# Kernel tuning notes

Hardware: AMD Instinct MI355X
Metric: run time of the kernel (lower is better)

The kernel has to match this reference:

```python
import jax, jax.numpy as jnp
import numpy as np

MAX_OBJECTS = 20
NODE_FEAT_DIM = 16
HID = 256
N_OPS = 8
N_COLORS = 10
B = 16384
EPS = 1e-5


def _ln(x, g, b):
    m = x.mean(-1, keepdims=True)
    v = ((x - m) ** 2).mean(-1, keepdims=True)
    return (x - m) / jnp.sqrt(v + EPS) * g + b


def _mlp(x, w1, b1, w2, b2):
    return jax.nn.relu(x @ w1 + b1) @ w2 + b2


def setup_inputs() -> dict:
    key = jax.random.key(0)
    ks = jax.random.split(key, 32)
    w = lambda k, shp: (jax.random.normal(k, shp, jnp.float32) * 0.02)
    return {
        "nf": jax.random.normal(ks[0], (B, MAX_OBJECTS, NODE_FEAT_DIM), jnp.float32),
        "nn_c": jax.random.randint(ks[1], (B,), 0, MAX_OBJECTS),
        "neW": w(ks[2], (NODE_FEAT_DIM, HID)), "neb": jnp.zeros((HID,), jnp.float32),
        "g1W1": w(ks[3], (2 * HID, HID)), "g1b1": jnp.zeros((HID,), jnp.float32),
        "g1W2": w(ks[4], (HID, HID)), "g1b2": jnp.zeros((HID,), jnp.float32),
        "g2W1": w(ks[5], (2 * HID, HID)), "g2b1": jnp.zeros((HID,), jnp.float32),
        "g2W2": w(ks[6], (HID, HID)), "g2b2": jnp.zeros((HID,), jnp.float32),
        "n1g": jnp.ones((HID,), jnp.float32), "n1b": jnp.zeros((HID,), jnp.float32),
        "n2g": jnp.ones((HID,), jnp.float32), "n2b": jnp.zeros((HID,), jnp.float32),
        "ohW": w(ks[7], (HID, N_OPS)), "ohb": jnp.zeros((N_OPS,), jnp.float32),
        "c1W": w(ks[8], (HID, N_COLORS)), "c1b": jnp.zeros((N_COLORS,), jnp.float32),
        "c2W": w(ks[9], (HID, N_COLORS)), "c2b": jnp.zeros((N_COLORS,), jnp.float32),
        "pqW": w(ks[10], (HID, HID)), "pqb": jnp.zeros((HID,), jnp.float32),
        "pkW": w(ks[11], (HID, HID)), "pkb": jnp.zeros((HID,), jnp.float32),
    }


def reference(nf, nn_c, neW, neb, g1W1, g1b1, g1W2, g1b2, g2W1, g2b1, g2W2, g2b2,
              n1g, n1b, n2g, n2b, ohW, ohb, c1W, c1b, c2W, c2b, pqW, pqb, pkW, pkb):
    mask = jnp.arange(MAX_OBJECTS)[None, :] < nn_c[:, None]  # [B, N]
    mf = mask.astype(jnp.float32)[..., None]                 # [B, N, 1]
    denom = jnp.clip(mf.sum(1, keepdims=True), 1.0)          # [B, 1, 1]

    h = nf @ neW + neb                                       # [B, N, H]
    msg = (h * mf).sum(1, keepdims=True) / denom             # [B, 1, H]
    h = h + _mlp(jnp.concatenate([h, jnp.broadcast_to(msg, h.shape)], -1), g1W1, g1b1, g1W2, g1b2)
    h = _ln(h, n1g, n1b) * mf

    msg = (h * mf).sum(1, keepdims=True) / denom
    h = h + _mlp(jnp.concatenate([h, jnp.broadcast_to(msg, h.shape)], -1), g2W1, g2b1, g2W2, g2b2)
    h = _ln(h, n2g, n2b) * mf

    g = (h * mf).sum(1) / jnp.clip(mf.sum(1), 1.0)           # [B, H]

    q = g @ pqW + pqb                                        # [B, H]
    k = h @ pkW + pkb                                        # [B, N, H]
    pl = jnp.einsum('bh,bnh->bn', q, k)
    pl = jnp.where(mask, pl, -1e9)
    return (g @ ohW + ohb, g @ c1W + c1b, g @ c2W + c2b, pl)
```

## Files before the change

### kernel.cpp

```cpp
#include <hip/hip_runtime.h>

typedef unsigned char u8;
typedef unsigned int  u32;
using f32x4 = __attribute__((ext_vector_type(4))) float;

#define DI __device__ __forceinline__

DI u32 pk4f8(float a, float b, float c, float d){
  int w = __builtin_amdgcn_cvt_pk_fp8_f32(a, b, 0, false);
  w = __builtin_amdgcn_cvt_pk_fp8_f32(c, d, w, true);
  return (u32)w;
}
DI u8 enc1(float a){
  return (u8)(__builtin_amdgcn_cvt_pk_fp8_f32(a, a, 0, false) & 0xFF);
}
DI float dc0(u32 v){ return __builtin_amdgcn_cvt_f32_fp8((int)v, 0); }
DI float dc1(u32 v){ return __builtin_amdgcn_cvt_f32_fp8((int)v, 1); }
DI float dc2(u32 v){ return __builtin_amdgcn_cvt_f32_fp8((int)v, 2); }
DI float dc3(u32 v){ return __builtin_amdgcn_cvt_f32_fp8((int)v, 3); }

DI f32x4 MFMA8(long a, long b, f32x4 c){
  return __builtin_amdgcn_mfma_f32_16x16x32_fp8_fp8(a, b, c, 0, 0, 0);
}

DI int swz8(int row, int col){ return (row << 8) + (col ^ ((row & 15) << 3)); }
DI long ldsA8(const u8* buf, int row, int k0){ return *(const long*)(buf + swz8(row, k0)); }
DI long ldG8(const u8* p){ return *(const long*)p; }

DI long mk8(float v0, float v1, float v2, float v3, float v4, float v5, float v6, float v7){
  u32 lo = pk4f8(v0, v1, v2, v3), hi = pk4f8(v4, v5, v6, v7);
  return (long)(((unsigned long long)hi << 32) | (unsigned long long)lo);
}
DI long loadW8T(const float* __restrict__ W, int n, int k0){
  return mk8(W[(k0+0)*256+n]*8.f, W[(k0+1)*256+n]*8.f, W[(k0+2)*256+n]*8.f, W[(k0+3)*256+n]*8.f,
             W[(k0+4)*256+n]*8.f, W[(k0+5)*256+n]*8.f, W[(k0+6)*256+n]*8.f, W[(k0+7)*256+n]*8.f);
}
DI long loadW8T16(const float* __restrict__ W, int n, int k0){
  float v[8];
#pragma unroll
  for (int j = 0; j < 8; j++){ int k = k0 + j; v[j] = (k < 16) ? W[k*256+n]*8.f : 0.f; }
  return mk8(v[0],v[1],v[2],v[3],v[4],v[5],v[6],v[7]);
}
DI long loadW8row(const float* __restrict__ W, int n, int k0){
  const float* p = W + n*256 + k0;
  return mk8(p[0]*8.f,p[1]*8.f,p[2]*8.f,p[3]*8.f,p[4]*8.f,p[5]*8.f,p[6]*8.f,p[7]*8.f);
}

#define WS_NEWT  0
#define WS_W1AT1 8192
#define WS_W1BT1 73728
#define WS_W2T1  139264
#define WS_W1AT2 204800
#define WS_W1BT2 270336
#define WS_W2T2  335872
#define WS_PQWT  401408
#define WS_PKWP  466944
#define WS_TOTAL 532480

__global__ void prep_weights(
    const float* __restrict__ neW, const float* __restrict__ g1W1,
    const float* __restrict__ g1W2, const float* __restrict__ g2W1,
    const float* __restrict__ g2W2, const float* __restrict__ pqW,
    const float* __restrict__ pkW, u8* __restrict__ ws)
{
  int i = blockIdx.x * 256 + threadIdx.x;
  if (i >= WS_TOTAL) return;
  float v;
  if (i < 8192){
    int n = i >> 5, k = i & 31;
    v = (k < 16) ? neW[k * 256 + n] : 0.0f;
  } else {
    int j = i - 8192;
    int region = j >> 16;
    int idx = j & 65535;
    int n = idx >> 8, k = idx & 255;
    switch (region){
      case 0: v = g1W1[k * 256 + n]; break;
      case 1: v = g1W1[(256 + k) * 256 + n]; break;
      case 2: v = g1W2[k * 256 + n]; break;
      case 3: v = g2W1[k * 256 + n]; break;
      case 4: v = g2W1[(256 + k) * 256 + n]; break;
      case 5: v = g2W2[k * 256 + n]; break;
      case 6: v = pqW[k * 256 + n]; break;
      default: v = pkW[idx]; break;
    }
  }
  ws[i] = enc1(v * 8.0f);
}

template<bool PREPPED>
__global__ __launch_bounds__(256, 3) void fused_graphnet(
    const float* __restrict__ nf, const int* __restrict__ nn_c,
    const float* __restrict__ neW, const float* __restrict__ neb,
    const float* __restrict__ g1W1, const float* __restrict__ g1b1,
    const float* __restrict__ g1W2, const float* __restrict__ g1b2,
    const float* __restrict__ g2W1, const float* __restrict__ g2b1,
    const float* __restrict__ g2W2, const float* __restrict__ g2b2,
    const float* __restrict__ n1g, const float* __restrict__ n1b,
    const float* __restrict__ n2g, const float* __restrict__ n2b,
    const float* __restrict__ ohW, const float* __restrict__ ohb,
    const float* __restrict__ c1W, const float* __restrict__ c1b,
    const float* __restrict__ c2W, const float* __restrict__ c2b,
    const float* __restrict__ pqW, const float* __restrict__ pqb,
    const float* __restrict__ pkW, const float* __restrict__ pkb,
    const u8* __restrict__ ws, float* __restrict__ out,
    int out_n, int Bv)
{
  __shared__ __align__(16) u8 bufA[80 * 256];
  __shared__ __align__(16) u8 bufB[80 * 256];
  __shared__ __align__(16) u8 smallA[8 * 256];
  __shared__ float pbf[4 * 256];
  __shared__ float rowstats[4][80][2];
  __shared__ float qdot[4];
  __shared__ int   cntS[4];
  __shared__ float dinvS[4];

  const int b0 = blockIdx.x * 4;
  const int tid = threadIdx.x;
  const int wave = tid >> 6, lane = tid & 63;
  const int lg = lane >> 4, lc = lane & 15;
  const int n0 = wave * 64;

  const int Bout = out_n / 48;
  const int off_c1 = 8 * Bout;
  const int off_c2 = 18 * Bout;
  const int off_pl = 28 * Bout;

  if (tid < 4){
    int bi = b0 + tid; if (bi >= Bv) bi = Bv - 1;
    int c = nn_c[bi];
    c = c < 0 ? 0 : (c > 20 ? 20 : c);
    cntS[tid] = c;
    dinvS[tid] = 1.0f / (float)(c < 1 ? 1 : c);
  }

  for (int i = tid; i < 80 * 4; i += 256){
    int row = i >> 2, c0 = 16 + (i & 3) * 4;
    *(u32*)(bufB + swz8(row, c0)) = 0u;
  }
  for (int i = tid; i < 80 * 4; i += 256){
    int row = i >> 2, k0 = (i & 3) * 4;
    int gr = b0 * 20 + row; if (gr >= Bv * 20) gr = Bv * 20 - 1;
    const float* p = nf + gr * 16 + k0;
    *(u32*)(bufB + swz8(row, k0)) = pk4f8(p[0], p[1], p[2], p[3]);
  }
  __syncthreads();

  const f32x4 zero4 = {0.0f, 0.0f, 0.0f, 0.0f};

#pragma unroll 1
  for (int nh = 0; nh < 2; nh++){
    const int n0h = n0 + nh * 32;
    f32x4 acc[5][2];
#pragma unroll
    for (int mt = 0; mt < 5; mt++){
      long a = ldsA8(bufB, mt * 16 + lc, lg * 8);
#pragma unroll
      for (int nt = 0; nt < 2; nt++){
        int n = n0h + nt * 16 + lc;
        long bfr;
        if constexpr (PREPPED) bfr = ldG8(ws + WS_NEWT + n * 32 + lg * 8);
        else bfr = loadW8T16(neW, n, lg * 8);
        acc[mt][nt] = MFMA8(a, bfr, zero4);
      }
    }
#pragma unroll
    for (int nt = 0; nt < 2; nt++){
      float bb = neb[n0h + nt * 16 + lc];
#pragma unroll
      for (int mt = 0; mt < 5; mt++)
#pragma unroll
        for (int r = 0; r < 4; r++){
          int row = mt * 16 + lg * 4 + r;
          int col = n0h + nt * 16 + lc;
          bufA[swz8(row, col)] = enc1(acc[mt][nt][r] * 0.125f + bb);
        }
    }
  }
  __syncthreads();

  for (int rd = 0; rd < 2; rd++){
    const int w1at = (rd == 0) ? WS_W1AT1 : WS_W1AT2;
    const int w1bt = (rd == 0) ? WS_W1BT1 : WS_W1BT2;
    const int w2t  = (rd == 0) ? WS_W2T1  : WS_W2T2;
    const float* W1 = (rd == 0) ? g1W1 : g2W1;
    const float* W2 = (rd == 0) ? g1W2 : g2W2;
    const float* b1p = (rd == 0) ? g1b1 : g2b1;
    const float* b2p = (rd == 0) ? g1b2 : g2b2;
    const float* ngp = (rd == 0) ? n1g : n2g;
    const float* nbp = (rd == 0) ? n1b : n2b;

    {
      int b = tid >> 6;
      int c0 = (tid & 63) * 4;
      int c = cntS[b];
      float s0 = 0, s1 = 0, s2 = 0, s3 = 0;
      for (int r = 0; r < c; r++){
        u32 v = *(const u32*)(bufA + swz8(b * 20 + r, c0));
        s0 += dc0(v); s1 += dc1(v); s2 += dc2(v); s3 += dc3(v);
      }
      float di = dinvS[b];
      *(u32*)(smallA + swz8(b, c0)) = pk4f8(s0 * di, s1 * di, s2 * di, s3 * di);
    }
    __syncthreads();

#pragma unroll 1
    for (int nh = 0; nh < 2; nh++){
      const int n0h = n0 + nh * 32;
      f32x4 acc[2];
#pragma unroll
      for (int nt = 0; nt < 2; nt++) acc[nt] = zero4;
#pragma unroll 1
      for (int kk = 0; kk < 8; kk++){
        long a = ldsA8(smallA, lc & 3, kk * 32 + lg * 8);
#pragma unroll
        for (int nt = 0; nt < 2; nt++){
          int n = n0h + nt * 16 + lc;
          long bfr;
          if constexpr (PREPPED) bfr = ldG8(ws + w1bt + n * 256 + kk * 32 + lg * 8);
          else bfr = loadW8T(W1 + 256 * 256, n, kk * 32 + lg * 8);
          acc[nt] = MFMA8(a, bfr, acc[nt]);
        }
      }
      if (lg == 0){
#pragma unroll
        for (int nt = 0; nt < 2; nt++)
#pragma unroll
          for (int r = 0; r < 4; r++){
            int col = n0h + nt * 16 + lc;
            pbf[r * 256 + col] = acc[nt][r] * 0.125f + b1p[col];
          }
      }
    }

#pragma unroll 1
    for (int nh = 0; nh < 2; nh++){
      const int n0h = n0 + nh * 32;
      f32x4 tacc[5][2];
#pragma unroll
      for (int mt = 0; mt < 5; mt++)
#pragma unroll
        for (int nt = 0; nt < 2; nt++) tacc[mt][nt] = zero4;
#pragma unroll 1
      for (int kk = 0; kk < 8; kk++){
#pragma unroll
        for (int mt = 0; mt < 5; mt++){
          long a = ldsA8(bufA, mt * 16 + lc, kk * 32 + lg * 8);
#pragma unroll
          for (int nt = 0; nt < 2; nt++){
            int n = n0h + nt * 16 + lc;
            long bfr;
            if constexpr (PREPPED) bfr = ldG8(ws + w1at + n * 256 + kk * 32 + lg * 8);
            else bfr = loadW8T(W1, n, kk * 32 + lg * 8);
            tacc[mt][nt] = MFMA8(a, bfr, tacc[mt][nt]);
          }
        }
      }
#pragma unroll
      for (int mt = 0; mt < 5; mt++)
#pragma unroll
        for (int nt = 0; nt < 2; nt++)
#pragma unroll
          for (int r = 0; r < 4; r++){
            int row = mt * 16 + lg * 4 + r;
            int col = n0h + nt * 16 + lc;
            float v = tacc[mt][nt][r] * 0.125f + pbf[(row / 20) * 256 + col];
            bufB[swz8(row, col)] = enc1(fmaxf(v, 0.0f));
          }
    }
    __syncthreads();

#pragma unroll 1
    for (int nh = 0; nh < 2; nh++){
      const int n0h = n0 + nh * 32;
      f32x4 tacc[5][2];
#pragma unroll
      for (int mt = 0; mt < 5; mt++)
#pragma unroll
        for (int nt = 0; nt < 2; nt++) tacc[mt][nt] = zero4;
#pragma unroll 1
      for (int kk = 0; kk < 8; kk++){
#pragma unroll
        for (int mt = 0; mt < 5; mt++){
          long a = ldsA8(bufB, mt * 16 + lc, kk * 32 + lg * 8);
#pragma unroll
          for (int nt = 0; nt < 2; nt++){
            int n = n0h + nt * 16 + lc;
            long bfr;
            if constexpr (PREPPED) bfr = ldG8(ws + w2t + n * 256 + kk * 32 + lg * 8);
            else bfr = loadW8T(W2, n, kk * 32 + lg * 8);
            tacc[mt][nt] = MFMA8(a, bfr, tacc[mt][nt]);
          }
        }
      }
#pragma unroll
      for (int nt = 0; nt < 2; nt++){
        float b2s = b2p[n0h + nt * 16 + lc];
#pragma unroll
        for (int mt = 0; mt < 5; mt++)
#pragma unroll
          for (int r = 0; r < 4; r++){
            int row = mt * 16 + lg * 4 + r;
            int col = n0h + nt * 16 + lc;
            u32 rv = bufA[swz8(row, col)];
            float v = tacc[mt][nt][r] * 0.125f + dc0(rv) + b2s;
            bufA[swz8(row, col)] = enc1(v);
          }
      }
    }

    {
#pragma unroll
      for (int mt = 0; mt < 5; mt++)
#pragma unroll
        for (int r = 0; r < 4; r++){
          int row = mt * 16 + lg * 4 + r;
          float s1 = 0, s2 = 0;
#pragma unroll
          for (int nt = 0; nt < 4; nt++){
            float v = dc0((u32)bufA[swz8(row, n0 + nt * 16 + lc)]);
            s1 += v; s2 += v * v;
          }
#pragma unroll
          for (int d = 1; d < 16; d <<= 1){ s1 += __shfl_xor(s1, d, 64); s2 += __shfl_xor(s2, d, 64); }
          if (lc == 0){ rowstats[wave][row][0] = s1; rowstats[wave][row][1] = s2; }
        }
      __syncthreads();

      float ngv[4], nbv[4];
#pragma unroll
      for (int nt = 0; nt < 4; nt++){
        ngv[nt] = ngp[n0 + nt * 16 + lc];
        nbv[nt] = nbp[n0 + nt * 16 + lc];
      }
#pragma unroll
      for (int mt = 0; mt < 5; mt++)
#pragma unroll
        for (int r = 0; r < 4; r++){
          int row = mt * 16 + lg * 4 + r;
          float t1s = rowstats[0][row][0] + rowstats[1][row][0] + rowstats[2][row][0] + rowstats[3][row][0];
          float t2s = rowstats[0][row][1] + rowstats[1][row][1] + rowstats[2][row][1] + rowstats[3][row][1];
          float mean = t1s * (1.0f / 256.0f);
          float var  = t2s * (1.0f / 256.0f) - mean * mean;
          float rstd = rsqrtf(fmaxf(var, 0.0f) + 1e-5f);
          int bb = row / 20;
          float mf = ((row - bb * 20) < cntS[bb]) ? 1.0f : 0.0f;
#pragma unroll
          for (int nt = 0; nt < 4; nt++){
            int col = n0 + nt * 16 + lc;
            float v = dc0((u32)bufA[swz8(row, col)]);
            bufA[swz8(row, col)] = enc1(((v - mean) * rstd * ngv[nt] + nbv[nt]) * mf);
          }
        }
    }
    __syncthreads();
  }

  {
    int b = tid >> 6;
    int c0 = (tid & 63) * 4;
    int c = cntS[b];
    float s0 = 0, s1 = 0, s2 = 0, s3 = 0;
    for (int r = 0; r < c; r++){
      u32 v = *(const u32*)(bufA + swz8(b * 20 + r, c0));
      s0 += dc0(v); s1 += dc1(v); s2 += dc2(v); s3 += dc3(v);
    }
    float di = dinvS[b];
    *(u32*)(smallA + swz8(b, c0)) = pk4f8(s0 * di, s1 * di, s2 * di, s3 * di);
  }
  __syncthreads();

  {
    f32x4 qacc[4];
#pragma unroll
    for (int nt = 0; nt < 4; nt++) qacc[nt] = zero4;
#pragma unroll 1
    for (int kk = 0; kk < 8; kk++){
      long a = ldsA8(smallA, lc & 3, kk * 32 + lg * 8);
#pragma unroll
      for (int nt = 0; nt < 4; nt++){
        int n = n0 + nt * 16 + lc;
        long bfr;
        if constexpr (PREPPED) bfr = ldG8(ws + WS_PQWT + n * 256 + kk * 32 + lg * 8);
        else bfr = loadW8T(pqW, n, kk * 32 + lg * 8);
        qacc[nt] = MFMA8(a, bfr, qacc[nt]);
      }
    }
    if (lg == 0){
#pragma unroll
      for (int nt = 0; nt < 4; nt++)
#pragma unroll
        for (int r = 0; r < 4; r++){
          int col = n0 + nt * 16 + lc;
          smallA[swz8(4 + r, col)] = enc1(qacc[nt][r] * 0.125f + pqb[col]);
        }
    }
  }
  __syncthreads();

  {
    u32 qv = *(const u32*)(smallA + swz8(4 + wave, lane * 4));
    float p = dc0(qv) * pkb[lane * 4 + 0] + dc1(qv) * pkb[lane * 4 + 1]
            + dc2(qv) * pkb[lane * 4 + 2] + dc3(qv) * pkb[lane * 4 + 3];
#pragma unroll
    for (int d = 1; d < 64; d <<= 1) p += __shfl_xor(p, d, 64);
    if (lane == 0) qdot[wave] = p;
  }

  {
    f32x4 racc[4];
#pragma unroll
    for (int nt = 0; nt < 4; nt++) racc[nt] = zero4;
#pragma unroll 1
    for (int kk = 0; kk < 8; kk++){
      long a = ldsA8(smallA, 4 + (lc & 3), kk * 32 + lg * 8);
#pragma unroll
      for (int nt = 0; nt < 4; nt++){
        int n = n0 + nt * 16 + lc;
        long bfr;
        if constexpr (PREPPED) bfr = ldG8(ws + WS_PKWP + n * 256 + kk * 32 + lg * 8);
        else bfr = loadW8row(pkW, n, kk * 32 + lg * 8);
        racc[nt] = MFMA8(a, bfr, racc[nt]);
      }
    }
    if (lg == 0){
#pragma unroll
      for (int nt = 0; nt < 4; nt++)
#pragma unroll
        for (int r = 0; r < 4; r++)
          pbf[r * 256 + (n0 + nt * 16 + lc)] = racc[nt][r] * 0.125f;
    }
  }
  __syncthreads();

  {
    const int b = wave;
    if (b0 + b < Bv){
      int cb = cntS[b];
      float qd = qdot[b];
      for (int rr = 0; rr < 20; rr++){
        int row = b * 20 + rr;
        u32 hv = *(const u32*)(bufA + swz8(row, lane * 4));
        const float* rp = pbf + b * 256 + lane * 4;
        float p = dc0(hv) * rp[0] + dc1(hv) * rp[1] + dc2(hv) * rp[2] + dc3(hv) * rp[3];
#pragma unroll
        for (int d = 1; d < 64; d <<= 1) p += __shfl_xor(p, d, 64);
        if (lane == 0){
          float v = (rr < cb) ? (p + qd) : -1e9f;
          out[off_pl + (b0 + b) * 20 + rr] = v;
        }
      }
    }
  }

  {
    const int b = wave;
    if (b0 + b < Bv){
      u32 gv = *(const u32*)(smallA + swz8(b, lane * 4));
      float g0 = dc0(gv), g1 = dc1(gv), g2 = dc2(gv), g3 = dc3(gv);
#pragma unroll 1
      for (int o = 0; o < 28; o++){
        const float* W; const float* bias; int ncol, col, off;
        if (o < 8)      { W = ohW; bias = ohb; ncol = 8;  col = o;      off = 0; }
        else if (o < 18){ W = c1W; bias = c1b; ncol = 10; col = o - 8;  off = off_c1; }
        else            { W = c2W; bias = c2b; ncol = 10; col = o - 18; off = off_c2; }
        int k = lane * 4;
        float p = g0 * W[(k + 0) * ncol + col] + g1 * W[(k + 1) * ncol + col]
                + g2 * W[(k + 2) * ncol + col] + g3 * W[(k + 3) * ncol + col];
#pragma unroll
        for (int d = 1; d < 64; d <<= 1) p += __shfl_xor(p, d, 64);
        if (lane == 0) out[off + (b0 + b) * ncol + col] = p + bias[col];
      }
    }
  }
}

extern "C" void kernel_launch(void* const* d_in, const int* in_sizes, int n_in,
                              void* d_out, int out_size, void* d_ws, size_t ws_size,
                              hipStream_t stream)
{
  const float* nf   = (const float*)d_in[0];
  const int*   nn_c = (const int*)d_in[1];
  const float* neW  = (const float*)d_in[2];
  const float* neb  = (const float*)d_in[3];
  const float* g1W1 = (const float*)d_in[4];
  const float* g1b1 = (const float*)d_in[5];
  const float* g1W2 = (const float*)d_in[6];
  const float* g1b2 = (const float*)d_in[7];
  const float* g2W1 = (const float*)d_in[8];
  const float* g2b1 = (const float*)d_in[9];
  const float* g2W2 = (const float*)d_in[10];
  const float* g2b2 = (const float*)d_in[11];
  const float* n1g  = (const float*)d_in[12];
  const float* n1b  = (const float*)d_in[13];
  const float* n2g  = (const float*)d_in[14];
  const float* n2b  = (const float*)d_in[15];
  const float* ohW  = (const float*)d_in[16];
  const float* ohb  = (const float*)d_in[17];
  const float* c1W  = (const float*)d_in[18];
  const float* c1b  = (const float*)d_in[19];
  const float* c2W  = (const float*)d_in[20];
  const float* c2b  = (const float*)d_in[21];
  const float* pqW  = (const float*)d_in[22];
  const float* pqb  = (const float*)d_in[23];
  const float* pkW  = (const float*)d_in[24];
  const float* pkb  = (const float*)d_in[25];

  float* outp = (float*)d_out;
  u8* ws = (u8*)d_ws;
  int B = in_sizes[0] / 320;
  int grid = (B + 3) / 4;

  if (ws_size >= (size_t)WS_TOTAL){
    prep_weights<<<(WS_TOTAL + 255) / 256, 256, 0, stream>>>(
        neW, g1W1, g1W2, g2W1, g2W2, pqW, pkW, ws);
    fused_graphnet<true><<<grid, 256, 0, stream>>>(
        nf, nn_c, neW, neb, g1W1, g1b1, g1W2, g1b2, g2W1, g2b1, g2W2, g2b2,
        n1g, n1b, n2g, n2b, ohW, ohb, c1W, c1b, c2W, c2b, pqW, pqb, pkW, pkb,
        ws, outp, out_size, B);
  } else {
    fused_graphnet<false><<<grid, 256, 0, stream>>>(
        nf, nn_c, neW, neb, g1W1, g1b1, g1W2, g1b2, g2W1, g2b1, g2W2, g2b2,
        n1g, n1b, n2g, n2b, ohW, ohb, c1W, c1b, c2W, c2b, pqW, pqb, pkW, pkb,
        ws, outp, out_size, B);
  }
}
```

Before: 916.3 us.

## Split work across 8 waves per block and software-prefetch weight fragments

Doubles the block to 512 threads so each wave owns 32 output columns instead of looping over two 32-column halves. The LayerNorm row statistics are reduced across 8 waves, and the small gather/head phases are divided between waves 0-3 and 4-7. The W1/W2 inner k-loops now prefetch the next k-slice of weight fragments from global memory one iteration ahead. This aims to hide global weight-load latency and raise wave-level parallelism. The cost is more registers per thread under the new launch bounds and more threads contending for the same shared-memory footprint.

```diff
diff --git a/kernel.cpp b/kernel.cpp
--- a/kernel.cpp
+++ b/kernel.cpp
@@ -89,7 +89,7 @@
 }
 
 template<bool PREPPED>
-__global__ __launch_bounds__(256, 3) void fused_graphnet(
+__global__ __launch_bounds__(512, 4) void fused_graphnet(
     const float* __restrict__ nf, const int* __restrict__ nn_c,
     const float* __restrict__ neW, const float* __restrict__ neb,
     const float* __restrict__ g1W1, const float* __restrict__ g1b1,
@@ -110,7 +110,7 @@
   __shared__ __align__(16) u8 bufB[80 * 256];
   __shared__ __align__(16) u8 smallA[8 * 256];
   __shared__ float pbf[4 * 256];
-  __shared__ float rowstats[4][80][2];
+  __shared__ float rowstats[8][80][2];
   __shared__ float qdot[4];
   __shared__ int   cntS[4];
   __shared__ float dinvS[4];
@@ -119,7 +119,7 @@
   const int tid = threadIdx.x;
   const int wave = tid >> 6, lane = tid & 63;
   const int lg = lane >> 4, lc = lane & 15;
-  const int n0 = wave * 64;
+  const int n0 = wave * 32;
 
   const int Bout = out_n / 48;
   const int off_c1 = 8 * Bout;
@@ -134,11 +134,11 @@
     dinvS[tid] = 1.0f / (float)(c < 1 ? 1 : c);
   }
 
-  for (int i = tid; i < 80 * 4; i += 256){
+  for (int i = tid; i < 80 * 4; i += 512){
     int row = i >> 2, c0 = 16 + (i & 3) * 4;
     *(u32*)(bufB + swz8(row, c0)) = 0u;
   }
-  for (int i = tid; i < 80 * 4; i += 256){
+  for (int i = tid; i < 80 * 4; i += 512){
     int row = i >> 2, k0 = (i & 3) * 4;
     int gr = b0 * 20 + row; if (gr >= Bv * 20) gr = Bv * 20 - 1;
     const float* p = nf + gr * 16 + k0;
@@ -148,16 +148,14 @@
 
   const f32x4 zero4 = {0.0f, 0.0f, 0.0f, 0.0f};
 
-#pragma unroll 1
-  for (int nh = 0; nh < 2; nh++){
-    const int n0h = n0 + nh * 32;
+  {
     f32x4 acc[5][2];
 #pragma unroll
     for (int mt = 0; mt < 5; mt++){
       long a = ldsA8(bufB, mt * 16 + lc, lg * 8);
 #pragma unroll
       for (int nt = 0; nt < 2; nt++){
-        int n = n0h + nt * 16 + lc;
+        int n = n0 + nt * 16 + lc;
         long bfr;
         if constexpr (PREPPED) bfr = ldG8(ws + WS_NEWT + n * 32 + lg * 8);
         else bfr = loadW8T16(neW, n, lg * 8);
@@ -166,13 +164,13 @@
     }
 #pragma unroll
     for (int nt = 0; nt < 2; nt++){
-      float bb = neb[n0h + nt * 16 + lc];
+      float bb = neb[n0 + nt * 16 + lc];
 #pragma unroll
       for (int mt = 0; mt < 5; mt++)
 #pragma unroll
         for (int r = 0; r < 4; r++){
           int row = mt * 16 + lg * 4 + r;
-          int col = n0h + nt * 16 + lc;
+          int col = n0 + nt * 16 + lc;
           bufA[swz8(row, col)] = enc1(acc[mt][nt][r] * 0.125f + bb);
         }
     }
@@ -190,7 +188,7 @@
     const float* ngp = (rd == 0) ? n1g : n2g;
     const float* nbp = (rd == 0) ? n1b : n2b;
 
-    {
+    if (tid < 256){
       int b = tid >> 6;
       int c0 = (tid & 63) * 4;
       int c = cntS[b];
@@ -204,56 +202,66 @@
     }
     __syncthreads();
 
-#pragma unroll 1
-    for (int nh = 0; nh < 2; nh++){
-      const int n0h = n0 + nh * 32;
+    {
       f32x4 acc[2];
 #pragma unroll
       for (int nt = 0; nt < 2; nt++) acc[nt] = zero4;
+      long bp0, bp1;
+      {
+        int n_0 = n0 + lc, n_1 = n0 + 16 + lc;
+        if constexpr (PREPPED){ bp0 = ldG8(ws + w1bt + n_0 * 256 + lg * 8); bp1 = ldG8(ws + w1bt + n_1 * 256 + lg * 8); }
+        else { bp0 = loadW8T(W1 + 256 * 256, n_0, lg * 8); bp1 = loadW8T(W1 + 256 * 256, n_1, lg * 8); }
+      }
 #pragma unroll 1
       for (int kk = 0; kk < 8; kk++){
+        long bn0 = bp0, bn1 = bp1;
+        if (kk < 7){
+          int k1 = (kk + 1) * 32 + lg * 8;
+          int n_0 = n0 + lc, n_1 = n0 + 16 + lc;
+          if constexpr (PREPPED){ bp0 = ldG8(ws + w1bt + n_0 * 256 + k1); bp1 = ldG8(ws + w1bt + n_1 * 256 + k1); }
+          else { bp0 = loadW8T(W1 + 256 * 256, n_0, k1); bp1 = loadW8T(W1 + 256 * 256, n_1, k1); }
+        }
         long a = ldsA8(smallA, lc & 3, kk * 32 + lg * 8);
-#pragma unroll
-        for (int nt = 0; nt < 2; nt++){
-          int n = n0h + nt * 16 + lc;
-          long bfr;
-          if constexpr (PREPPED) bfr = ldG8(ws + w1bt + n * 256 + kk * 32 + lg * 8);
-          else bfr = loadW8T(W1 + 256 * 256, n, kk * 32 + lg * 8);
-          acc[nt] = MFMA8(a, bfr, acc[nt]);
-        }
+        acc[0] = MFMA8(a, bn0, acc[0]);
+        acc[1] = MFMA8(a, bn1, acc[1]);
       }
       if (lg == 0){
 #pragma unroll
         for (int nt = 0; nt < 2; nt++)
 #pragma unroll
           for (int r = 0; r < 4; r++){
-            int col = n0h + nt * 16 + lc;
+            int col = n0 + nt * 16 + lc;
             pbf[r * 256 + col] = acc[nt][r] * 0.125f + b1p[col];
           }
       }
     }
 
-#pragma unroll 1
-    for (int nh = 0; nh < 2; nh++){
-      const int n0h = n0 + nh * 32;
+    {
       f32x4 tacc[5][2];
 #pragma unroll
       for (int mt = 0; mt < 5; mt++)
 #pragma unroll
         for (int nt = 0; nt < 2; nt++) tacc[mt][nt] = zero4;
+      long bp0, bp1;
+      {
+        int n_0 = n0 + lc, n_1 = n0 + 16 + lc;
+        if constexpr (PREPPED){ bp0 = ldG8(ws + w1at + n_0 * 256 + lg * 8); bp1 = ldG8(ws + w1at + n_1 * 256 + lg * 8); }
+        else { bp0 = loadW8T(W1, n_0, lg * 8); bp1 = loadW8T(W1, n_1, lg * 8); }
+      }
 #pragma unroll 1
       for (int kk = 0; kk < 8; kk++){
+        long bn0 = bp0, bn1 = bp1;
+        if (kk < 7){
+          int k1 = (kk + 1) * 32 + lg * 8;
+          int n_0 = n0 + lc, n_1 = n0 + 16 + lc;
+          if constexpr (PREPPED){ bp0 = ldG8(ws + w1at + n_0 * 256 + k1); bp1 = ldG8(ws + w1at + n_1 * 256 + k1); }
+          else { bp0 = loadW8T(W1, n_0, k1); bp1 = loadW8T(W1, n_1, k1); }
+        }
 #pragma unroll
         for (int mt = 0; mt < 5; mt++){
           long a = ldsA8(bufA, mt * 16 + lc, kk * 32 + lg * 8);
-#pragma unroll
-          for (int nt = 0; nt < 2; nt++){
-            int n = n0h + nt * 16 + lc;
-            long bfr;
-            if constexpr (PREPPED) bfr = ldG8(ws + w1at + n * 256 + kk * 32 + lg * 8);
-            else bfr = loadW8T(W1, n, kk * 32 + lg * 8);
-            tacc[mt][nt] = MFMA8(a, bfr, tacc[mt][nt]);
-          }
+          tacc[mt][0] = MFMA8(a, bn0, tacc[mt][0]);
+          tacc[mt][1] = MFMA8(a, bn1, tacc[mt][1]);
         }
       }
 #pragma unroll
@@ -263,45 +271,50 @@
 #pragma unroll
           for (int r = 0; r < 4; r++){
             int row = mt * 16 + lg * 4 + r;
-            int col = n0h + nt * 16 + lc;
+            int col = n0 + nt * 16 + lc;
             float v = tacc[mt][nt][r] * 0.125f + pbf[(row / 20) * 256 + col];
             bufB[swz8(row, col)] = enc1(fmaxf(v, 0.0f));
           }
     }
     __syncthreads();
 
-#pragma unroll 1
-    for (int nh = 0; nh < 2; nh++){
-      const int n0h = n0 + nh * 32;
+    {
       f32x4 tacc[5][2];
 #pragma unroll
       for (int mt = 0; mt < 5; mt++)
 #pragma unroll
         for (int nt = 0; nt < 2; nt++) tacc[mt][nt] = zero4;
+      long bp0, bp1;
+      {
+        int n_0 = n0 + lc, n_1 = n0 + 16 + lc;
+        if constexpr (PREPPED){ bp0 = ldG8(ws + w2t + n_0 * 256 + lg * 8); bp1 = ldG8(ws + w2t + n_1 * 256 + lg * 8); }
+        else { bp0 = loadW8T(W2, n_0, lg * 8); bp1 = loadW8T(W2, n_1, lg * 8); }
+      }
 #pragma unroll 1
       for (int kk = 0; kk < 8; kk++){
+        long bn0 = bp0, bn1 = bp1;
+        if (kk < 7){
+          int k1 = (kk + 1) * 32 + lg * 8;
+          int n_0 = n0 + lc, n_1 = n0 + 16 + lc;
+          if constexpr (PREPPED){ bp0 = ldG8(ws + w2t + n_0 * 256 + k1); bp1 = ldG8(ws + w2t + n_1 * 256 + k1); }
+          else { bp0 = loadW8T(W2, n_0, k1); bp1 = loadW8T(W2, n_1, k1); }
+        }
 #pragma unroll
         for (int mt = 0; mt < 5; mt++){
           long a = ldsA8(bufB, mt * 16 + lc, kk * 32 + lg * 8);
-#pragma unroll
-          for (int nt = 0; nt < 2; nt++){
-            int n = n0h + nt * 16 + lc;
-            long bfr;
-            if constexpr (PREPPED) bfr = ldG8(ws + w2t + n * 256 + kk * 32 + lg * 8);
-            else bfr = loadW8T(W2, n, kk * 32 + lg * 8);
-            tacc[mt][nt] = MFMA8(a, bfr, tacc[mt][nt]);
-          }
+          tacc[mt][0] = MFMA8(a, bn0, tacc[mt][0]);
+          tacc[mt][1] = MFMA8(a, bn1, tacc[mt][1]);
         }
       }
 #pragma unroll
       for (int nt = 0; nt < 2; nt++){
-        float b2s = b2p[n0h + nt * 16 + lc];
+        float b2s = b2p[n0 + nt * 16 + lc];
 #pragma unroll
         for (int mt = 0; mt < 5; mt++)
 #pragma unroll
           for (int r = 0; r < 4; r++){
             int row = mt * 16 + lg * 4 + r;
-            int col = n0h + nt * 16 + lc;
+            int col = n0 + nt * 16 + lc;
             u32 rv = bufA[swz8(row, col)];
             float v = tacc[mt][nt][r] * 0.125f + dc0(rv) + b2s;
             bufA[swz8(row, col)] = enc1(v);
@@ -317,7 +330,7 @@
           int row = mt * 16 + lg * 4 + r;
           float s1 = 0, s2 = 0;
 #pragma unroll
-          for (int nt = 0; nt < 4; nt++){
+          for (int nt = 0; nt < 2; nt++){
             float v = dc0((u32)bufA[swz8(row, n0 + nt * 16 + lc)]);
             s1 += v; s2 += v * v;
           }
@@ -327,36 +340,31 @@
         }
       __syncthreads();
 
-      float ngv[4], nbv[4];
-#pragma unroll
-      for (int nt = 0; nt < 4; nt++){
-        ngv[nt] = ngp[n0 + nt * 16 + lc];
-        nbv[nt] = nbp[n0 + nt * 16 + lc];
-      }
 #pragma unroll
       for (int mt = 0; mt < 5; mt++)
 #pragma unroll
         for (int r = 0; r < 4; r++){
           int row = mt * 16 + lg * 4 + r;
-          float t1s = rowstats[0][row][0] + rowstats[1][row][0] + rowstats[2][row][0] + rowstats[3][row][0];
-          float t2s = rowstats[0][row][1] + rowstats[1][row][1] + rowstats[2][row][1] + rowstats[3][row][1];
+          float t1s = 0, t2s = 0;
+#pragma unroll
+          for (int w = 0; w < 8; w++){ t1s += rowstats[w][row][0]; t2s += rowstats[w][row][1]; }
           float mean = t1s * (1.0f / 256.0f);
           float var  = t2s * (1.0f / 256.0f) - mean * mean;
           float rstd = rsqrtf(fmaxf(var, 0.0f) + 1e-5f);
           int bb = row / 20;
           float mf = ((row - bb * 20) < cntS[bb]) ? 1.0f : 0.0f;
 #pragma unroll
-          for (int nt = 0; nt < 4; nt++){
+          for (int nt = 0; nt < 2; nt++){
             int col = n0 + nt * 16 + lc;
             float v = dc0((u32)bufA[swz8(row, col)]);
-            bufA[swz8(row, col)] = enc1(((v - mean) * rstd * ngv[nt] + nbv[nt]) * mf);
+            bufA[swz8(row, col)] = enc1(((v - mean) * rstd * ngp[col] + nbp[col]) * mf);
           }
         }
     }
     __syncthreads();
   }
 
-  {
+  if (tid < 256){
     int b = tid >> 6;
     int c0 = (tid & 63) * 4;
     int c = cntS[b];
@@ -371,14 +379,14 @@
   __syncthreads();
 
   {
-    f32x4 qacc[4];
-#pragma unroll
-    for (int nt = 0; nt < 4; nt++) qacc[nt] = zero4;
+    f32x4 qacc[2];
+#pragma unroll
+    for (int nt = 0; nt < 2; nt++) qacc[nt] = zero4;
 #pragma unroll 1
     for (int kk = 0; kk < 8; kk++){
       long a = ldsA8(smallA, lc & 3, kk * 32 + lg * 8);
 #pragma unroll
-      for (int nt = 0; nt < 4; nt++){
+      for (int nt = 0; nt < 2; nt++){
         int n = n0 + nt * 16 + lc;
         long bfr;
         if constexpr (PREPPED) bfr = ldG8(ws + WS_PQWT + n * 256 + kk * 32 + lg * 8);
@@ -388,7 +396,7 @@
     }
     if (lg == 0){
 #pragma unroll
-      for (int nt = 0; nt < 4; nt++)
+      for (int nt = 0; nt < 2; nt++)
 #pragma unroll
         for (int r = 0; r < 4; r++){
           int col = n0 + nt * 16 + lc;
@@ -398,7 +406,7 @@
   }
   __syncthreads();
 
-  {
+  if (wave < 4){
     u32 qv = *(const u32*)(smallA + swz8(4 + wave, lane * 4));
     float p = dc0(qv) * pkb[lane * 4 + 0] + dc1(qv) * pkb[lane * 4 + 1]
             + dc2(qv) * pkb[lane * 4 + 2] + dc3(qv) * pkb[lane * 4 + 3];
@@ -408,14 +416,14 @@
   }
 
   {
-    f32x4 racc[4];
-#pragma unroll
-    for (int nt = 0; nt < 4; nt++) racc[nt] = zero4;
+    f32x4 racc[2];
+#pragma unroll
+    for (int nt = 0; nt < 2; nt++) racc[nt] = zero4;
 #pragma unroll 1
     for (int kk = 0; kk < 8; kk++){
       long a = ldsA8(smallA, 4 + (lc & 3), kk * 32 + lg * 8);
 #pragma unroll
-      for (int nt = 0; nt < 4; nt++){
+      for (int nt = 0; nt < 2; nt++){
         int n = n0 + nt * 16 + lc;
         long bfr;
         if constexpr (PREPPED) bfr = ldG8(ws + WS_PKWP + n * 256 + kk * 32 + lg * 8);
@@ -425,7 +433,7 @@
     }
     if (lg == 0){
 #pragma unroll
-      for (int nt = 0; nt < 4; nt++)
+      for (int nt = 0; nt < 2; nt++)
 #pragma unroll
         for (int r = 0; r < 4; r++)
           pbf[r * 256 + (n0 + nt * 16 + lc)] = racc[nt][r] * 0.125f;
@@ -433,7 +441,7 @@
   }
   __syncthreads();
 
-  {
+  if (wave < 4){
     const int b = wave;
     if (b0 + b < Bv){
       int cb = cntS[b];
@@ -451,10 +459,8 @@
         }
       }
     }
-  }
-
-  {
-    const int b = wave;
+  } else {
+    const int b = wave - 4;
     if (b0 + b < Bv){
       u32 gv = *(const u32*)(smallA + swz8(b, lane * 4));
       float g0 = dc0(gv), g1 = dc1(gv), g2 = dc2(gv), g3 = dc3(gv);
@@ -514,12 +520,12 @@
   if (ws_size >= (size_t)WS_TOTAL){
     prep_weights<<<(WS_TOTAL + 255) / 256, 256, 0, stream>>>(
         neW, g1W1, g1W2, g2W1, g2W2, pqW, pkW, ws);
-    fused_graphnet<true><<<grid, 256, 0, stream>>>(
+    fused_graphnet<true><<<grid, 512, 0, stream>>>(
         nf, nn_c, neW, neb, g1W1, g1b1, g1W2, g1b2, g2W1, g2b1, g2W2, g2b2,
         n1g, n1b, n2g, n2b, ohW, ohb, c1W, c1b, c2W, c2b, pqW, pqb, pkW, pkb,
         ws, outp, out_size, B);
   } else {
-    fused_graphnet<false><<<grid, 256, 0, stream>>>(
+    fused_graphnet<false><<<grid, 512, 0, stream>>>(
         nf, nn_c, neW, neb, g1W1, g1b1, g1W2, g1b2, g2W1, g2b1, g2W2, g2b2,
         n1g, n1b, n2g, n2b, ohW, ohb, c1W, c1b, c2W, c2b, pqW, pqb, pkW, pkb,
         ws, outp, out_size, B);
```

Result: slower. 1.033 ms (+12.7%).
